# Optimization experiments

Measured on AMD Instinct MI355X. Metric: run time of the kernel, lower is better.

## Reference

```python
import jax, jax.numpy as jnp
import numpy as np

NBINS = 256


def setup_inputs() -> dict:
    key = jax.random.key(0)
    x = jax.random.uniform(key, (16, 3, 1024, 1024), dtype=jnp.float32)
    return {"x": x}


def reference(x):
    b, c, h, w = x.shape
    n = b * c
    xf = x.reshape(n, h * w)                      # (n, N) per-channel rows

    # global min/max over the whole tensor (matches torch.histogram range)
    mn = xf.min()
    mx = xf.max()
    span = mx - mn

    # per-row histogram via scatter-add; last bin is right-closed like torch.histogram
    scale = NBINS / span
    idx = jnp.clip(jnp.floor((xf - mn) * scale).astype(jnp.int32), 0, NBINS - 1)
    flat_idx = (jnp.arange(n, dtype=jnp.int32)[:, None] * NBINS + idx).reshape(-1)
    hist = jax.ops.segment_sum(
        jnp.ones((n * h * w,), dtype=jnp.float32), flat_idx,
        num_segments=n * NBINS,
    ).reshape(n, NBINS)
    hist = hist / hist.sum(axis=1, keepdims=True)  # normalized histograms

    # vectorized Otsu: cumulative weights/means -> inter-class variance
    t = jnp.arange(NBINS, dtype=hist.dtype)
    w_bg = jnp.cumsum(hist, axis=1)               # background weight up to t
    s_bg = jnp.cumsum(hist * t, axis=1)           # background weighted sum
    total = s_bg[:, -1:]                          # sum_i i*hist[i]
    w_fg = 1.0 - w_bg
    valid = (w_bg > 0) & (w_fg > 0)
    mean_bg = s_bg / jnp.where(w_bg > 0, w_bg, 1.0)
    mean_fg = (total - s_bg) / jnpp_safe(w_fg) if False else (total - s_bg) / jnp.where(w_fg > 0, w_fg, 1.0)
    var = jnp.where(valid, w_bg * w_fg * (mean_bg - mean_fg) ** 2, -jnp.inf)
    t_opt = jnp.argmax(var, axis=1)               # first max, like strict `>` loop

    # threshold = right edge of the optimal bin
    edges = mn + span * (jnp.arange(NBINS + 1, dtype=x.dtype) / NBINS)
    thresh = edges[t_opt + 1]                     # (n,)

    out = jnp.where(xf <= thresh[:, None], jnp.zeros((), x.dtype), xf)
    return out.reshape(b, c, h, w)
```

## Files before the change

kernel.cpp:

```cpp
#include <hip/hip_runtime.h>
#include <stdint.h>

#define NBINS 256
#define HW_SHIFT 20
#define HW4_SHIFT 18
#define BLOCK 256
#define NCOPY 16
#define MM_BLOCKS 2048
#define HIST_BLOCKS 1536
#define CHUNKS_PER_IMG 32
#define CHUNK4 8192
#define APPLY_BLOCKS 2048

typedef float nfloat4 __attribute__((ext_vector_type(4)));

__device__ __forceinline__ unsigned enc_f(float f) {
    unsigned u = __float_as_uint(f);
    return u ^ ((unsigned)((int)u >> 31) | 0x80000000u);
}


__global__ void __launch_bounds__(BLOCK)
k_minmax(const float4* __restrict__ x, float2* __restrict__ bmm, long n4) {
    float mn = __builtin_inff(), mx = -__builtin_inff();
    const long stride = (long)gridDim.x * BLOCK;
    long i = (long)blockIdx.x * BLOCK + threadIdx.x;
    for (; i + 3 * stride < n4; i += 4 * stride) {
        float4 a = x[i];
        float4 b = x[i + stride];
        float4 c = x[i + 2 * stride];
        float4 d = x[i + 3 * stride];
        mn = fminf(mn, fminf(fminf(a.x, a.y), fminf(a.z, a.w)));
        mx = fmaxf(mx, fmaxf(fmaxf(a.x, a.y), fmaxf(a.z, a.w)));
        mn = fminf(mn, fminf(fminf(b.x, b.y), fminf(b.z, b.w)));
        mx = fmaxf(mx, fmaxf(fmaxf(b.x, b.y), fmaxf(b.z, b.w)));
        mn = fminf(mn, fminf(fminf(c.x, c.y), fminf(c.z, c.w)));
        mx = fmaxf(mx, fmaxf(fmaxf(c.x, c.y), fmaxf(c.z, c.w)));
        mn = fminf(mn, fminf(fminf(d.x, d.y), fminf(d.z, d.w)));
        mx = fmaxf(mx, fmaxf(fmaxf(d.x, d.y), fmaxf(d.z, d.w)));
    }
    for (; i < n4; i += stride) {
        float4 a = x[i];
        mn = fminf(mn, fminf(fminf(a.x, a.y), fminf(a.z, a.w)));
        mx = fmaxf(mx, fmaxf(fmaxf(a.x, a.y), fmaxf(a.z, a.w)));
    }
    for (int off = 32; off; off >>= 1) {
        mn = fminf(mn, __shfl_down(mn, off));
        mx = fmaxf(mx, __shfl_down(mx, off));
    }
    __shared__ float smn[4], smx[4];
    int lane = threadIdx.x & 63, wv = threadIdx.x >> 6;
    if (lane == 0) { smn[wv] = mn; smx[wv] = mx; }
    __syncthreads();
    if (threadIdx.x == 0) {
        for (int j = 1; j < BLOCK / 64; j++) {
            mn = fminf(mn, smn[j]); mx = fmaxf(mx, smx[j]);
        }
        bmm[blockIdx.x] = make_float2(mn, mx);
    }
}

__device__ __forceinline__ void reduce_bmm(const float2* __restrict__ bmm,
                                           unsigned* sh_u, float* omn, float* omx) {
    float mn = __builtin_inff(), mx = -__builtin_inff();
    for (int j = threadIdx.x; j < MM_BLOCKS; j += BLOCK) {
        float2 v = bmm[j];
        mn = fminf(mn, v.x); mx = fmaxf(mx, v.y);
    }
    for (int off = 32; off; off >>= 1) {
        mn = fminf(mn, __shfl_down(mn, off));
        mx = fmaxf(mx, __shfl_down(mx, off));
    }
    int lane = threadIdx.x & 63, wv = threadIdx.x >> 6;
    if (lane == 0) { sh_u[2 * wv] = __float_as_uint(mn); sh_u[2 * wv + 1] = __float_as_uint(mx); }
    __syncthreads();
    if (threadIdx.x == 0) {
        for (int j = 1; j < BLOCK / 64; j++) {
            mn = fminf(mn, __uint_as_float(sh_u[2 * j]));
            mx = fmaxf(mx, __uint_as_float(sh_u[2 * j + 1]));
        }
        sh_u[0] = __float_as_uint(mn); sh_u[1] = __float_as_uint(mx);
    }
    __syncthreads();
    *omn = __uint_as_float(sh_u[0]);
    *omx = __uint_as_float(sh_u[1]);
    __syncthreads();
}

__global__ void __launch_bounds__(BLOCK)
k_hist(const float4* __restrict__ x, const float2* __restrict__ bmm,
       unsigned* __restrict__ partial, int nimg) {
    __shared__ unsigned sh[NBINS * NCOPY];
    float mn, mx;
    reduce_bmm(bmm, sh, &mn, &mx);
    float span = mx - mn;
    float scale = __fdiv_rn(256.0f, span);

    const int nchunks = nimg * CHUNKS_PER_IMG;
    const int tid = threadIdx.x;
    const int c = tid & (NCOPY - 1);
    for (int chunk = blockIdx.x; chunk < nchunks; chunk += HIST_BLOCKS) {
        for (int i = tid; i < NBINS * NCOPY; i += BLOCK) sh[i] = 0u;
        __syncthreads();
        const float4* base = x + ((long)(chunk >> 5) << HW4_SHIFT)
                               + (long)(chunk & (CHUNKS_PER_IMG - 1)) * CHUNK4;
        for (int i = tid; i < CHUNK4; i += 4 * BLOCK) {
            float4 v0 = base[i];
            float4 v1 = base[i + BLOCK];
            float4 v2 = base[i + 2 * BLOCK];
            float4 v3 = base[i + 3 * BLOCK];
            int b0 = (int)floorf((v0.x - mn) * scale);
            int b1 = (int)floorf((v0.y - mn) * scale);
            int b2 = (int)floorf((v0.z - mn) * scale);
            int b3 = (int)floorf((v0.w - mn) * scale);
            int b4 = (int)floorf((v1.x - mn) * scale);
            int b5 = (int)floorf((v1.y - mn) * scale);
            int b6 = (int)floorf((v1.z - mn) * scale);
            int b7 = (int)floorf((v1.w - mn) * scale);
            int b8 = (int)floorf((v2.x - mn) * scale);
            int b9 = (int)floorf((v2.y - mn) * scale);
            int ba = (int)floorf((v2.z - mn) * scale);
            int bb = (int)floorf((v2.w - mn) * scale);
            int bc = (int)floorf((v3.x - mn) * scale);
            int bd = (int)floorf((v3.y - mn) * scale);
            int be = (int)floorf((v3.z - mn) * scale);
            int bf = (int)floorf((v3.w - mn) * scale);
            b0 = min(max(b0, 0), NBINS - 1); b1 = min(max(b1, 0), NBINS - 1);
            b2 = min(max(b2, 0), NBINS - 1); b3 = min(max(b3, 0), NBINS - 1);
            b4 = min(max(b4, 0), NBINS - 1); b5 = min(max(b5, 0), NBINS - 1);
            b6 = min(max(b6, 0), NBINS - 1); b7 = min(max(b7, 0), NBINS - 1);
            b8 = min(max(b8, 0), NBINS - 1); b9 = min(max(b9, 0), NBINS - 1);
            ba = min(max(ba, 0), NBINS - 1); bb = min(max(bb, 0), NBINS - 1);
            bc = min(max(bc, 0), NBINS - 1); bd = min(max(bd, 0), NBINS - 1);
            be = min(max(be, 0), NBINS - 1); bf = min(max(bf, 0), NBINS - 1);
            atomicAdd(&sh[b0 * NCOPY + c], 1u);
            atomicAdd(&sh[b1 * NCOPY + c], 1u);
            atomicAdd(&sh[b2 * NCOPY + c], 1u);
            atomicAdd(&sh[b3 * NCOPY + c], 1u);
            atomicAdd(&sh[b4 * NCOPY + c], 1u);
            atomicAdd(&sh[b5 * NCOPY + c], 1u);
            atomicAdd(&sh[b6 * NCOPY + c], 1u);
            atomicAdd(&sh[b7 * NCOPY + c], 1u);
            atomicAdd(&sh[b8 * NCOPY + c], 1u);
            atomicAdd(&sh[b9 * NCOPY + c], 1u);
            atomicAdd(&sh[ba * NCOPY + c], 1u);
            atomicAdd(&sh[bb * NCOPY + c], 1u);
            atomicAdd(&sh[bc * NCOPY + c], 1u);
            atomicAdd(&sh[bd * NCOPY + c], 1u);
            atomicAdd(&sh[be * NCOPY + c], 1u);
            atomicAdd(&sh[bf * NCOPY + c], 1u);
        }
        __syncthreads();
        unsigned sum = 0;
        #pragma unroll
        for (int k = 0; k < NCOPY; k++) {
            int cc = (k + tid) & (NCOPY - 1);
            sum += sh[tid * NCOPY + cc];
        }
        partial[(long)chunk * NBINS + tid] = sum;
        __syncthreads();
    }
}

__global__ void __launch_bounds__(BLOCK)
k_otsu(const unsigned* __restrict__ partial, const float2* __restrict__ bmm,
       float* __restrict__ thresh) {
    __shared__ unsigned sh[3 * NBINS + 8];
    float mn, mx;
    reduce_bmm(bmm, sh, &mn, &mx);

    const int img = blockIdx.x;
    const int tid = threadIdx.x;
    const unsigned* p = partial + (long)img * CHUNKS_PER_IMG * NBINS;
    unsigned hsum = 0;
    #pragma unroll 4
    for (int k = 0; k < CHUNKS_PER_IMG; k++) hsum += p[k * NBINS + tid];
    sh[tid] = hsum;
    __syncthreads();
    if (tid == 0) {
        const float inv_total = 1.0f / 1048576.0f;
        float ww = 0.0f, ss = 0.0f;
        for (int t = 0; t < NBINS; t++) {
            float pp = __fmul_rn((float)sh[t], inv_total);
            ww = __fadd_rn(ww, pp);
            ss = __fadd_rn(ss, __fmul_rn(pp, (float)t));
            sh[NBINS + t] = __float_as_uint(ww);
            sh[2 * NBINS + t] = __float_as_uint(ss);
        }
    }
    __syncthreads();
    float total = __uint_as_float(sh[3 * NBINS - 1]);
    float ww = __uint_as_float(sh[NBINS + tid]);
    float ss = __uint_as_float(sh[2 * NBINS + tid]);
    float wf = __fsub_rn(1.0f, ww);
    float var;
    if (ww > 0.0f && wf > 0.0f) {
        float mb = __fdiv_rn(ss, ww);
        float mf = __fdiv_rn(__fsub_rn(total, ss), wf);
        float d = __fsub_rn(mb, mf);
        var = __fmul_rn(__fmul_rn(ww, wf), __fmul_rn(d, d));
    } else {
        var = -__builtin_inff();
    }
    unsigned long long key = ((unsigned long long)enc_f(var) << 32)
                           | (unsigned)(NBINS - 1 - tid);
    for (int off = 32; off; off >>= 1) {
        unsigned long long o = __shfl_down(key, off);
        key = key > o ? key : o;
    }
    int lane = tid & 63, wv = tid >> 6;
    if (lane == 0) {
        sh[3 * NBINS + 2 * wv] = (unsigned)(key & 0xFFFFFFFFull);
        sh[3 * NBINS + 2 * wv + 1] = (unsigned)(key >> 32);
    }
    __syncthreads();
    if (tid == 0) {
        for (int j = 1; j < BLOCK / 64; j++) {
            unsigned long long o = ((unsigned long long)sh[3 * NBINS + 2 * j + 1] << 32)
                                 | sh[3 * NBINS + 2 * j];
            key = key > o ? key : o;
        }
        int bestt = NBINS - 1 - (int)(key & 0xFFFFFFFFull);
        float sp = __fsub_rn(mx, mn);
        float q = __fmul_rn((float)(bestt + 1), 1.0f / 256.0f);
        thresh[img] = __fadd_rn(mn, __fmul_rn(sp, q));
    }
}

__global__ void __launch_bounds__(BLOCK)
k_apply(const float4* __restrict__ x, nfloat4* __restrict__ out,
        const float* __restrict__ thresh, long n4, int nimg) {
    __shared__ unsigned sth[NBINS];
    if (threadIdx.x < nimg) sth[threadIdx.x] = __float_as_uint(thresh[threadIdx.x]);
    __syncthreads();
    const long stride = (long)gridDim.x * BLOCK;
    long i = (long)blockIdx.x * BLOCK + threadIdx.x;
    for (; i + 3 * stride < n4; i += 4 * stride) {
        float4 v0 = x[i];
        float4 v1 = x[i + stride];
        float4 v2 = x[i + 2 * stride];
        float4 v3 = x[i + 3 * stride];
        float t0 = __uint_as_float(sth[(int)(i >> HW4_SHIFT)]);
        float t1 = __uint_as_float(sth[(int)((i + stride) >> HW4_SHIFT)]);
        float t2 = __uint_as_float(sth[(int)((i + 2 * stride) >> HW4_SHIFT)]);
        float t3 = __uint_as_float(sth[(int)((i + 3 * stride) >> HW4_SHIFT)]);
        nfloat4 o0, o1, o2, o3;
        o0.x = (v0.x <= t0) ? 0.0f : v0.x;
        o0.y = (v0.y <= t0) ? 0.0f : v0.y;
        o0.z = (v0.z <= t0) ? 0.0f : v0.z;
        o0.w = (v0.w <= t0) ? 0.0f : v0.w;
        o1.x = (v1.x <= t1) ? 0.0f : v1.x;
        o1.y = (v1.y <= t1) ? 0.0f : v1.y;
        o1.z = (v1.z <= t1) ? 0.0f : v1.z;
        o1.w = (v1.w <= t1) ? 0.0f : v1.w;
        o2.x = (v2.x <= t2) ? 0.0f : v2.x;
        o2.y = (v2.y <= t2) ? 0.0f : v2.y;
        o2.z = (v2.z <= t2) ? 0.0f : v2.z;
        o2.w = (v2.w <= t2) ? 0.0f : v2.w;
        o3.x = (v3.x <= t3) ? 0.0f : v3.x;
        o3.y = (v3.y <= t3) ? 0.0f : v3.y;
        o3.z = (v3.z <= t3) ? 0.0f : v3.z;
        o3.w = (v3.w <= t3) ? 0.0f : v3.w;
        __builtin_nontemporal_store(o0, &out[i]);
        __builtin_nontemporal_store(o1, &out[i + stride]);
        __builtin_nontemporal_store(o2, &out[i + 2 * stride]);
        __builtin_nontemporal_store(o3, &out[i + 3 * stride]);
    }
    for (; i < n4; i += stride) {
        float4 v0 = x[i];
        float t0 = __uint_as_float(sth[(int)(i >> HW4_SHIFT)]);
        nfloat4 o0;
        o0.x = (v0.x <= t0) ? 0.0f : v0.x;
        o0.y = (v0.y <= t0) ? 0.0f : v0.y;
        o0.z = (v0.z <= t0) ? 0.0f : v0.z;
        o0.w = (v0.w <= t0) ? 0.0f : v0.w;
        __builtin_nontemporal_store(o0, &out[i]);
    }
}

extern "C" void kernel_launch(void* const* d_in, const int* in_sizes, int n_in,
                              void* d_out, int out_size, void* d_ws, size_t ws_size,
                              hipStream_t stream) {
    const float4* x = (const float4*)d_in[0];
    nfloat4* out = (nfloat4*)d_out;
    long n = (long)in_sizes[0];
    long n4 = n >> 2;
    int nimg = (int)(n >> HW_SHIFT);

    float2* bmm = (float2*)d_ws;
    unsigned* partial = (unsigned*)((float*)d_ws + 2 * MM_BLOCKS);
    float* thresh = (float*)(partial + (long)nimg * CHUNKS_PER_IMG * NBINS);

    k_minmax<<<MM_BLOCKS, BLOCK, 0, stream>>>(x, bmm, n4);
    k_hist<<<HIST_BLOCKS, BLOCK, 0, stream>>>(x, bmm, partial, nimg);
    k_otsu<<<nimg, BLOCK, 0, stream>>>(partial, bmm, thresh);
    k_apply<<<APPLY_BLOCKS, BLOCK, 0, stream>>>(x, out, thresh, n4, nimg);
}
```

Measured before the change: 410.9 us.

## Fuse Otsu threshold computation into histogram kernel via last-block counter

After: 604.0 us. 1.47x slower.

```diff
diff --git a/kernel.cpp b/kernel.cpp
--- a/kernel.cpp
+++ b/kernel.cpp
@@ -21,7 +21,9 @@
 
 
 __global__ void __launch_bounds__(BLOCK)
-k_minmax(const float4* __restrict__ x, float2* __restrict__ bmm, long n4) {
+k_minmax(const float4* __restrict__ x, float2* __restrict__ bmm, long n4,
+         unsigned* __restrict__ cnt, int nimg) {
+    if (blockIdx.x == 0 && threadIdx.x < nimg) cnt[threadIdx.x] = 0u;
     float mn = __builtin_inff(), mx = -__builtin_inff();
     const long stride = (long)gridDim.x * BLOCK;
     long i = (long)blockIdx.x * BLOCK + threadIdx.x;
@@ -89,88 +91,90 @@
 
 __global__ void __launch_bounds__(BLOCK)
 k_hist(const float4* __restrict__ x, const float2* __restrict__ bmm,
-       unsigned* __restrict__ partial, int nimg) {
+       unsigned* __restrict__ partial, unsigned* __restrict__ cnt,
+       float* __restrict__ thresh, int nimg) {
     __shared__ unsigned sh[NBINS * NCOPY];
     float mn, mx;
     reduce_bmm(bmm, sh, &mn, &mx);
     float span = mx - mn;
     float scale = __fdiv_rn(256.0f, span);
 
-    const int nchunks = nimg * CHUNKS_PER_IMG;
     const int tid = threadIdx.x;
+    const int chunk = blockIdx.x;
+    const int img = chunk >> 5;
     const int c = tid & (NCOPY - 1);
-    for (int chunk = blockIdx.x; chunk < nchunks; chunk += HIST_BLOCKS) {
-        for (int i = tid; i < NBINS * NCOPY; i += BLOCK) sh[i] = 0u;
-        __syncthreads();
-        const float4* base = x + ((long)(chunk >> 5) << HW4_SHIFT)
-                               + (long)(chunk & (CHUNKS_PER_IMG - 1)) * CHUNK4;
-        for (int i = tid; i < CHUNK4; i += 4 * BLOCK) {
-            float4 v0 = base[i];
-            float4 v1 = base[i + BLOCK];
-            float4 v2 = base[i + 2 * BLOCK];
-            float4 v3 = base[i + 3 * BLOCK];
-            int b0 = (int)floorf((v0.x - mn) * scale);
-            int b1 = (int)floorf((v0.y - mn) * scale);
-            int b2 = (int)floorf((v0.z - mn) * scale);
-            int b3 = (int)floorf((v0.w - mn) * scale);
-            int b4 = (int)floorf((v1.x - mn) * scale);
-            int b5 = (int)floorf((v1.y - mn) * scale);
-            int b6 = (int)floorf((v1.z - mn) * scale);
-            int b7 = (int)floorf((v1.w - mn) * scale);
-            int b8 = (int)floorf((v2.x - mn) * scale);
-            int b9 = (int)floorf((v2.y - mn) * scale);
-            int ba = (int)floorf((v2.z - mn) * scale);
-            int bb = (int)floorf((v2.w - mn) * scale);
-            int bc = (int)floorf((v3.x - mn) * scale);
-            int bd = (int)floorf((v3.y - mn) * scale);
-            int be = (int)floorf((v3.z - mn) * scale);
-            int bf = (int)floorf((v3.w - mn) * scale);
-            b0 = min(max(b0, 0), NBINS - 1); b1 = min(max(b1, 0), NBINS - 1);
-            b2 = min(max(b2, 0), NBINS - 1); b3 = min(max(b3, 0), NBINS - 1);
-            b4 = min(max(b4, 0), NBINS - 1); b5 = min(max(b5, 0), NBINS - 1);
-            b6 = min(max(b6, 0), NBINS - 1); b7 = min(max(b7, 0), NBINS - 1);
-            b8 = min(max(b8, 0), NBINS - 1); b9 = min(max(b9, 0), NBINS - 1);
-            ba = min(max(ba, 0), NBINS - 1); bb = min(max(bb, 0), NBINS - 1);
-            bc = min(max(bc, 0), NBINS - 1); bd = min(max(bd, 0), NBINS - 1);
-            be = min(max(be, 0), NBINS - 1); bf = min(max(bf, 0), NBINS - 1);
-            atomicAdd(&sh[b0 * NCOPY + c], 1u);
-            atomicAdd(&sh[b1 * NCOPY + c], 1u);
-            atomicAdd(&sh[b2 * NCOPY + c], 1u);
-            atomicAdd(&sh[b3 * NCOPY + c], 1u);
-            atomicAdd(&sh[b4 * NCOPY + c], 1u);
-            atomicAdd(&sh[b5 * NCOPY + c], 1u);
-            atomicAdd(&sh[b6 * NCOPY + c], 1u);
-            atomicAdd(&sh[b7 * NCOPY + c], 1u);
-            atomicAdd(&sh[b8 * NCOPY + c], 1u);
-            atomicAdd(&sh[b9 * NCOPY + c], 1u);
-            atomicAdd(&sh[ba * NCOPY + c], 1u);
-            atomicAdd(&sh[bb * NCOPY + c], 1u);
-            atomicAdd(&sh[bc * NCOPY + c], 1u);
-            atomicAdd(&sh[bd * NCOPY + c], 1u);
-            atomicAdd(&sh[be * NCOPY + c], 1u);
-            atomicAdd(&sh[bf * NCOPY + c], 1u);
-        }
-        __syncthreads();
-        unsigned sum = 0;
-        #pragma unroll
-        for (int k = 0; k < NCOPY; k++) {
-            int cc = (k + tid) & (NCOPY - 1);
-            sum += sh[tid * NCOPY + cc];
-        }
-        partial[(long)chunk * NBINS + tid] = sum;
-        __syncthreads();
-    }
-}
-
-__global__ void __launch_bounds__(BLOCK)
-k_otsu(const unsigned* __restrict__ partial, const float2* __restrict__ bmm,
-       float* __restrict__ thresh) {
-    __shared__ unsigned sh[3 * NBINS + 8];
-    float mn, mx;
-    reduce_bmm(bmm, sh, &mn, &mx);
-
-    const int img = blockIdx.x;
-    const int tid = threadIdx.x;
+
+    for (int i = tid; i < NBINS * NCOPY; i += BLOCK) sh[i] = 0u;
+    __syncthreads();
+    const float4* base = x + ((long)img << HW4_SHIFT)
+                           + (long)(chunk & (CHUNKS_PER_IMG - 1)) * CHUNK4;
+    for (int i = tid; i < CHUNK4; i += 4 * BLOCK) {
+        float4 v0 = base[i];
+        float4 v1 = base[i + BLOCK];
+        float4 v2 = base[i + 2 * BLOCK];
+        float4 v3 = base[i + 3 * BLOCK];
+        int b0 = (int)floorf((v0.x - mn) * scale);
+        int b1 = (int)floorf((v0.y - mn) * scale);
+        int b2 = (int)floorf((v0.z - mn) * scale);
+        int b3 = (int)floorf((v0.w - mn) * scale);
+        int b4 = (int)floorf((v1.x - mn) * scale);
+        int b5 = (int)floorf((v1.y - mn) * scale);
+        int b6 = (int)floorf((v1.z - mn) * scale);
+        int b7 = (int)floorf((v1.w - mn) * scale);
+        int b8 = (int)floorf((v2.x - mn) * scale);
+        int b9 = (int)floorf((v2.y - mn) * scale);
+        int ba = (int)floorf((v2.z - mn) * scale);
+        int bb = (int)floorf((v2.w - mn) * scale);
+        int bc = (int)floorf((v3.x - mn) * scale);
+        int bd = (int)floorf((v3.y - mn) * scale);
+        int be = (int)floorf((v3.z - mn) * scale);
+        int bf = (int)floorf((v3.w - mn) * scale);
+        b0 = min(b0, NBINS - 1); b1 = min(b1, NBINS - 1);
+        b2 = min(b2, NBINS - 1); b3 = min(b3, NBINS - 1);
+        b4 = min(b4, NBINS - 1); b5 = min(b5, NBINS - 1);
+        b6 = min(b6, NBINS - 1); b7 = min(b7, NBINS - 1);
+        b8 = min(b8, NBINS - 1); b9 = min(b9, NBINS - 1);
+        ba = min(ba, NBINS - 1); bb = min(bb, NBINS - 1);
+        bc = min(bc, NBINS - 1); bd = min(bd, NBINS - 1);
+        be = min(be, NBINS - 1); bf = min(bf, NBINS - 1);
+        atomicAdd(&sh[b0 * NCOPY + c], 1u);
+        atomicAdd(&sh[b1 * NCOPY + c], 1u);
+        atomicAdd(&sh[b2 * NCOPY + c], 1u);
+        atomicAdd(&sh[b3 * NCOPY + c], 1u);
+        atomicAdd(&sh[b4 * NCOPY + c], 1u);
+        atomicAdd(&sh[b5 * NCOPY + c], 1u);
+        atomicAdd(&sh[b6 * NCOPY + c], 1u);
+        atomicAdd(&sh[b7 * NCOPY + c], 1u);
+        atomicAdd(&sh[b8 * NCOPY + c], 1u);
+        atomicAdd(&sh[b9 * NCOPY + c], 1u);
+        atomicAdd(&sh[ba * NCOPY + c], 1u);
+        atomicAdd(&sh[bb * NCOPY + c], 1u);
+        atomicAdd(&sh[bc * NCOPY + c], 1u);
+        atomicAdd(&sh[bd * NCOPY + c], 1u);
+        atomicAdd(&sh[be * NCOPY + c], 1u);
+        atomicAdd(&sh[bf * NCOPY + c], 1u);
+    }
+    __syncthreads();
+    unsigned sum = 0;
+    #pragma unroll
+    for (int k = 0; k < NCOPY; k++) {
+        int cc = (k + tid) & (NCOPY - 1);
+        sum += sh[tid * NCOPY + cc];
+    }
+    partial[(long)chunk * NBINS + tid] = sum;
+
+    __threadfence();
+    __syncthreads();
+    if (tid == 0) {
+        unsigned old = atomicAdd(&cnt[img], 1u);
+        sh[0] = (old == CHUNKS_PER_IMG - 1) ? 1u : 0u;
+    }
+    __syncthreads();
+    bool last = (sh[0] != 0u);
+    __syncthreads();
+    if (!last) return;
+    __threadfence();
+
     const unsigned* p = partial + (long)img * CHUNKS_PER_IMG * NBINS;
     unsigned hsum = 0;
     #pragma unroll 4
@@ -290,9 +294,9 @@
     float2* bmm = (float2*)d_ws;
     unsigned* partial = (unsigned*)((float*)d_ws + 2 * MM_BLOCKS);
     float* thresh = (float*)(partial + (long)nimg * CHUNKS_PER_IMG * NBINS);
-
-    k_minmax<<<MM_BLOCKS, BLOCK, 0, stream>>>(x, bmm, n4);
-    k_hist<<<HIST_BLOCKS, BLOCK, 0, stream>>>(x, bmm, partial, nimg);
-    k_otsu<<<nimg, BLOCK, 0, stream>>>(partial, bmm, thresh);
+    unsigned* cnt = (unsigned*)(thresh + nimg);
+
+    k_minmax<<<MM_BLOCKS, BLOCK, 0, stream>>>(x, bmm, n4, cnt, nimg);
+    k_hist<<<HIST_BLOCKS, BLOCK, 0, stream>>>(x, bmm, partial, cnt, thresh, nimg);
     k_apply<<<APPLY_BLOCKS, BLOCK, 0, stream>>>(x, out, thresh, n4, nimg);
 }
```
